# Kernel optimization log

Hardware: AMD Instinct MI355X
Metric: run time of the kernel (lower is better)

Reference implementation:

```python
import jax, jax.numpy as jnp
import numpy as np

T, B, H, V = 1024, 64, 256, 32000


def setup_inputs() -> dict:
    key = jax.random.key(0)
    ks = jax.random.split(key, 12)
    inputSequence = jax.random.randint(ks[0], (T, B), 0, V)
    lengths = jax.random.randint(ks[1], (B,), 1, T + 1)
    lengths = jnp.sort(lengths)[::-1]          # pack_padded_sequence needs descending
    lengths = lengths.at[0].set(T)             # max length == padded length
    s = 1.0 / np.sqrt(H)
    def w(k, shape):
        return jax.random.uniform(k, shape, jnp.float32, -s, s)
    return {
        "inputSequence": inputSequence,
        "inputLengths": lengths,
        "embedding": jax.random.normal(ks[2], (V, H), jnp.float32),
        "W_ih_f": w(ks[3], (3 * H, H)), "W_hh_f": w(ks[4], (3 * H, H)),
        "b_ih_f": w(ks[5], (3 * H,)),   "b_hh_f": w(ks[6], (3 * H,)),
        "W_ih_b": w(ks[7], (3 * H, H)), "W_hh_b": w(ks[8], (3 * H, H)),
        "b_ih_b": w(ks[9], (3 * H,)),   "b_hh_b": w(ks[10], (3 * H,)),
    }


def _gru_dir(emb, mask, Wih, Whh, bih, bhh, reverse):
    # emb: (T,B,H), mask: (T,B). PyTorch GRU cell math.
    Tn, Bn, Hn = emb.shape
    xg = emb @ Wih.T + bih                      # (T,B,3H) input-side gates precomputed
    def step(h, inp):
        xg_t, m = inp
        hg = h @ Whh.T + bhh                    # (B,3H)
        r = jax.nn.sigmoid(xg_t[:, :Hn] + hg[:, :Hn])
        z = jax.nn.sigmoid(xg_t[:, Hn:2 * Hn] + hg[:, Hn:2 * Hn])
        n = jnp.tanh(xg_t[:, 2 * Hn:] + r * hg[:, 2 * Hn:])
        h_new = (1.0 - z) * n + z * h
        m_ = m[:, None]
        h_next = jnp.where(m_, h_new, h)        # packed seq: frozen past length
        y = jnp.where(m_, h_new, 0.0)           # pad_packed zeros padded steps
        return h_next, y
    h0 = jnp.zeros((Bn, Hn), emb.dtype)
    hT, ys = jax.lax.scan(step, h0, (xg, mask), reverse=reverse)
    return ys, hT


def reference(inputSequence, inputLengths, embedding,
              W_ih_f, W_hh_f, b_ih_f, b_hh_f,
              W_ih_b, W_hh_b, b_ih_b, b_hh_b):
    Tn, Bn = inputSequence.shape
    emb = embedding[inputSequence]                              # (T,B,H)
    mask = jnp.arange(Tn)[:, None] < inputLengths[None, :]      # (T,B)
    yf, hf = _gru_dir(emb, mask, W_ih_f, W_hh_f, b_ih_f, b_hh_f, False)
    yb, hb = _gru_dir(emb, mask, W_ih_b, W_hh_b, b_ih_b, b_hh_b, True)
    outputs = yf + yb                                           # sum fwd/bwd halves
    hidden = jnp.stack([hf, hb], axis=0)                        # (2, B, H)
    return outputs, hidden
```

## Files before the change

kernel.cpp:

```cpp
#include <hip/hip_runtime.h>


typedef __attribute__((ext_vector_type(8))) short short8;
typedef __attribute__((ext_vector_type(4))) float floatx4;

__device__ __forceinline__ float rcp_(float x) { return __builtin_amdgcn_rcpf(x); }
__device__ __forceinline__ float sigmoid_(float x) { return rcp_(1.0f + __expf(-x)); }
__device__ __forceinline__ float tanh_(float x)    { return 1.0f - 2.0f * rcp_(1.0f + __expf(2.0f * x)); }
__device__ __forceinline__ unsigned short f2bf(float f) {
  unsigned int u = __float_as_uint(f);
  return (unsigned short)((u + 0x7fffu + ((u >> 16) & 1u)) >> 16);
}

__device__ __forceinline__ void ldsbar() {
  asm volatile("s_waitcnt lgkmcnt(0)" ::: "memory");
  __builtin_amdgcn_s_barrier();
  asm volatile("" ::: "memory");
}


__global__ __launch_bounds__(256) void prep_embB(
    const float* __restrict__ emb, unsigned short* __restrict__ embB) {
  int i4 = blockIdx.x * 256 + threadIdx.x;
  float4 v = ((const float4*)emb)[i4];
  ushort4 o;
  o.x = f2bf(v.x); o.y = f2bf(v.y); o.z = f2bf(v.z); o.w = f2bf(v.w);
  ((ushort4*)embB)[i4] = o;
}

__global__ __launch_bounds__(256) void prep_packB(
    const float* __restrict__ wf, const float* __restrict__ wb,
    unsigned short* __restrict__ oB) {
  int idx = blockIdx.x * 256 + threadIdx.x;
  int d = idx >= 196608;
  int o = idx - d * 196608;
  int jj   = o & 7;
  int lane = (o >> 3) & 63;
  int rest = o >> 9;
  int nt   = rest % 48;
  int kc   = rest / 48;
  int n = nt * 16 + (lane & 15);
  int k = kc * 32 + ((lane >> 4) << 3) + jj;
  const float* w = d ? wb : wf;
  oB[idx] = f2bf(w[n * 256 + k]);
}

__global__ __launch_bounds__(256) void prep_packA(
    const float* __restrict__ wf, const float* __restrict__ wb,
    unsigned short* __restrict__ oA) {
  int idx = blockIdx.x * 256 + threadIdx.x;
  int d = idx >= 196608;
  int o = idx - d * 196608;
  int jj   = o & 7;
  int lane = (o >> 3) & 63;
  int kc   = (o >> 9) & 7;
  int tl   = o >> 12;
  int row  = tl * 16 + (lane & 15);
  int k    = kc * 32 + ((lane >> 4) << 3) + jj;
  const float* w = d ? wb : wf;
  oA[idx] = f2bf(w[row * 256 + k]);
}

__global__ __launch_bounds__(512, 2) void fused_step(
    const int* __restrict__ seq, const int* __restrict__ lens,
    const unsigned short* __restrict__ embB,
    const unsigned short* __restrict__ pWihB,
    const unsigned short* __restrict__ pA,
    const float* __restrict__ bih_f, const float* __restrict__ bih_b,
    const float* __restrict__ bhh_f, const float* __restrict__ bhh_b,
    float* __restrict__ out, float* __restrict__ hcar,
    const float* __restrict__ xs_f, const float* __restrict__ xs_b,
    float* __restrict__ xw_f, float* __restrict__ xw_b,
    int nscan, int s_base_f, int s_base_b, int Tc, int is_last, int do_add,
    int xg_on, int x_base_f, int x_base_b) {
  __shared__ __align__(16) unsigned char smem[49152];
  const int bid = (int)blockIdx.x;
  const int tid = threadIdx.x;
  const int lane = tid & 63;

  if (bid < nscan) {
    __builtin_amdgcn_s_setprio(1);
    const int wv  = tid >> 6;
    const int qp  = bid >> 1;
    const int dir = bid & 1;
    const int b0  = qp * 2;

    const float* xg  = dir ? xs_b : xs_f;
    const float* bhh = dir ? bhh_b : bhh_f;
    const int len0 = lens[b0], len1 = lens[b0 + 1];
    const int lenmax = len0 > len1 ? len0 : len1;
    const int base = dir ? s_base_b : s_base_f;

    short8 af[6][8];
    {
      const short8* pA8 = (const short8*)(pA + (size_t)dir * 196608);
#pragma unroll
      for (int i = 0; i < 6; ++i) {
        const int tl = (i >> 1) * 16 + wv * 2 + (i & 1);
#pragma unroll
        for (int kc = 0; kc < 8; ++kc)
          af[i][kc] = pA8[((tl * 8 + kc) << 6) + lane];
      }
    }

    unsigned short* hbf = (unsigned short*)smem;
    float*          res = (float*)(smem + 2304);

    const int b  = lane >> 5;
    const int jj = lane & 31;
    const int j  = wv * 32 + jj;
    const int bb = b0 + b;
    const int blen = b ? len1 : len0;
    float hreg = hcar[dir * 16384 + bb * 256 + j];
    const float bhn = bhh[512 + j];
    hbf[b * 288 + j] = f2bf(hreg);
    __syncthreads();

    int s_lo, s_hi;
    if (dir == 0) { s_lo = 0; int e = lenmax - base; s_hi = e < 0 ? 0 : (e > Tc ? Tc : e); }
    else { int sk = base + Tc - lenmax; s_lo = sk < 0 ? 0 : (sk > Tc ? Tc : sk); s_hi = Tc; }

    const int nB = lane & 15, qq = lane >> 4;
    const bool bld = nB < 2;
    const unsigned short* hsrc0 = &hbf[nB * 288 + qq * 8];

    float xr = 0.f, xz = 0.f, xn = 0.f, oprev = 0.f;
    if (s_lo < s_hi) {
      const int t0  = dir ? (base + (Tc - 1 - s_lo)) : (base + s_lo);
      const float* xrow = xg + ((size_t)(t0 - base) * 64 + bb) * 768;
      xr = xrow[j]; xz = xrow[256 + j]; xn = xrow[512 + j];
      if (do_add) oprev = out[((size_t)t0 * 64 + bb) * 256 + j];
    }

    int p = 0;
    for (int s = s_lo; s < s_hi; ++s) {
      const int t  = dir ? (base + (Tc - 1 - s)) : (base + s);
      const bool act = t < blen;

      const int sn = (s + 1 < s_hi) ? s + 1 : s;
      const int tn = dir ? (base + (Tc - 1 - sn)) : (base + sn);
      float xr2, xz2, xn2, oprev2 = 0.f;
      {
        const float* xrow = xg + ((size_t)(tn - base) * 64 + bb) * 768;
        xr2 = xrow[j]; xz2 = xrow[256 + j]; xn2 = xrow[512 + j];
        if (do_add) oprev2 = out[((size_t)tn * 64 + bb) * 256 + j];
      }

      floatx4 acc[6];
#pragma unroll
      for (int i = 0; i < 6; ++i) acc[i] = (floatx4){0.f, 0.f, 0.f, 0.f};

      const unsigned short* hsrc = hsrc0 + p * 576;

      short8 b_cur = {0, 0, 0, 0, 0, 0, 0, 0};
      if (bld) b_cur = *(const short8*)(hsrc);
#pragma unroll
      for (int kc = 0; kc < 8; ++kc) {
        short8 b_nxt = {0, 0, 0, 0, 0, 0, 0, 0};
        if (kc < 7 && bld) b_nxt = *(const short8*)(hsrc + (kc + 1) * 32);
#pragma unroll
        for (int i = 0; i < 6; ++i)
          acc[i] = __builtin_amdgcn_mfma_f32_16x16x32_bf16(af[i][kc], b_cur, acc[i], 0, 0, 0);
        b_cur = b_nxt;
      }

      if (bld) {
#pragma unroll
        for (int i = 0; i < 6; ++i) {
          const int g = i >> 1, sub = i & 1;
          *(floatx4*)&res[(((wv * 3 + g) * 2 + nB) << 5) + sub * 16 + qq * 4] = acc[i];
        }
      }
      float ar = res[(((wv * 3 + 0) * 2 + b) << 5) + jj];
      float az = res[(((wv * 3 + 1) * 2 + b) << 5) + jj];
      float an = res[(((wv * 3 + 2) * 2 + b) << 5) + jj];

      float r  = sigmoid_(xr + ar);
      float z  = sigmoid_(xz + az);
      float nn = tanh_(xn + r * (an + bhn));
      float hn = (1.0f - z) * nn + z * hreg;
      if (act) hreg = hn;
      hbf[((p ^ 1) * 576) + b * 288 + j] = f2bf(hreg);
      if (act) out[((size_t)t * 64 + bb) * 256 + j] = do_add ? (oprev + hn) : hn;
      ldsbar();
      p ^= 1;

      xr = xr2; xz = xz2; xn = xn2; oprev = oprev2;
    }

    hcar[dir * 16384 + bb * 256 + j] = hreg;
    if (is_last)
      out[(size_t)1024 * 64 * 256 + (size_t)dir * 16384 + bb * 256 + j] = hreg;

  } else if (xg_on) {
    const int idx  = bid - nscan;
    const int sx   = idx >> 1;
    const int dir  = idx & 1;
    const int w    = tid >> 6;
    const int mt   = w & 3;
    const int h2   = w >> 2;
    const int t    = (dir ? x_base_b : x_base_f) + sx;
    const int c    = lane & 15, qq = lane >> 4;

    const float* bih = dir ? bih_b : bih_f;
    const float* bhh = dir ? bhh_b : bhh_f;
    float* xgo = (dir ? xw_b : xw_f) + (size_t)sx * 64 * 768;

    const int tk = seq[t * 64 + mt * 16 + c];
    const unsigned short* aptr = embB + (size_t)tk * 256 + qq * 8;
    short8 afr[8];
#pragma unroll
    for (int kc = 0; kc < 8; ++kc) afr[kc] = *(const short8*)(aptr + kc * 32);

    float4* Bs4 = (float4*)smem;

    floatx4 acc[24];
#pragma unroll
    for (int q = 0; q < 24; ++q) acc[q] = (floatx4){0.f, 0.f, 0.f, 0.f};

    for (int kc = 0; kc < 8; ++kc) {
      __syncthreads();
      const float4* src = (const float4*)(pWihB + (size_t)dir * 196608 + kc * 24576);
#pragma unroll
      for (int i = 0; i < 6; ++i) Bs4[tid + i * 512] = src[tid + i * 512];
      __syncthreads();
      const short8* bsv = (const short8*)Bs4;
      short8 af = afr[kc];
#pragma unroll
      for (int q = 0; q < 24; ++q) {
        int nt = h2 * 24 + q;
        acc[q] = __builtin_amdgcn_mfma_f32_16x16x32_bf16(af, bsv[nt * 64 + lane], acc[q], 0, 0, 0);
      }
    }

#pragma unroll
    for (int q = 0; q < 24; ++q) {
      int n = (h2 * 24 + q) * 16 + c;
      float bv = bih[n] + (n < 512 ? bhh[n] : 0.0f);
#pragma unroll
      for (int r = 0; r < 4; ++r)
        xgo[(size_t)(mt * 16 + qq * 4 + r) * 768 + n] = acc[q][r] + bv;
    }
  }
}

extern "C" void kernel_launch(void* const* d_in, const int* in_sizes, int n_in,
                              void* d_out, int out_size, void* d_ws, size_t ws_size,
                              hipStream_t stream) {
  const int*   seq   = (const int*)d_in[0];
  const int*   lens  = (const int*)d_in[1];
  const float* emb   = (const float*)d_in[2];
  const float* Wih_f = (const float*)d_in[3];
  const float* Whh_f = (const float*)d_in[4];
  const float* bih_f = (const float*)d_in[5];
  const float* bhh_f = (const float*)d_in[6];
  const float* Wih_b = (const float*)d_in[7];
  const float* Whh_b = (const float*)d_in[8];
  const float* bih_b = (const float*)d_in[9];
  const float* bhh_b = (const float*)d_in[10];
  float* out = (float*)d_out;
  float* ws  = (float*)d_ws;

  float*          hcar   = ws;
  unsigned short* pA     = (unsigned short*)(ws + 32768);
  unsigned short* pWihB  = (unsigned short*)(ws + 229376);
  unsigned short* embB   = (unsigned short*)(ws + 425984);
  float*          xgbase = ws + 4521984;

  int S[128], off[128], C = 0, Smax = 0;
  {
    size_t needA = (4521984ull + 4ull * 224ull * 49152ull) * 4ull;
    if (needA <= ws_size) {
      const int plan[6] = {64, 224, 224, 224, 224, 64};
      C = 6;
      for (int i = 0; i < C; ++i) S[i] = plan[i];
    } else {
      const int cands[7] = {512, 256, 128, 64, 32, 16, 8};
      int Tc = 8;
      for (int i = 0; i < 7; ++i) {
        size_t need = (4521984ull + 4ull * (size_t)cands[i] * 49152ull) * 4ull;
        if (need <= ws_size) { Tc = cands[i]; break; }
      }
      C = 1024 / Tc;
      for (int i = 0; i < C; ++i) S[i] = Tc;
    }
    int o = 0;
    for (int i = 0; i < C; ++i) { off[i] = o; o += S[i]; if (S[i] > Smax) Smax = S[i]; }
  }

  float* xb[2][2];
  for (int p = 0; p < 2; ++p)
    for (int d = 0; d < 2; ++d)
      xb[p][d] = xgbase + ((size_t)(p * 2 + d)) * Smax * 49152;

  hipMemsetAsync(d_out, 0, (size_t)1024 * 64 * 256 * 4, stream);
  hipMemsetAsync(hcar, 0, 32768ull * 4ull, stream);
  prep_embB<<<dim3(8000), dim3(256), 0, stream>>>(emb, embB);
  prep_packB<<<dim3(1536), dim3(256), 0, stream>>>(Wih_f, Wih_b, pWihB);
  prep_packA<<<dim3(1536), dim3(256), 0, stream>>>(Whh_f, Whh_b, pA);

  fused_step<<<dim3(2 * S[0]), dim3(512), 0, stream>>>(
      seq, lens, embB, pWihB, pA, bih_f, bih_b, bhh_f, bhh_b, out, hcar,
      xb[0][0], xb[0][1], xb[0][0], xb[0][1],
      0, 0, 0, S[0], 0, 0,
      1, off[0], off[C - 1]);

  for (int c = 0; c < C; ++c) {
    int xgon = (c + 1 < C) ? 1 : 0;
    int nblk = 64 + (xgon ? 2 * S[c + 1] : 0);
    fused_step<<<dim3(nblk), dim3(512), 0, stream>>>(
        seq, lens, embB, pWihB, pA, bih_f, bih_b, bhh_f, bhh_b, out, hcar,
        xb[c & 1][0], xb[c & 1][1], xb[(c + 1) & 1][0], xb[(c + 1) & 1][1],
        64, off[c], off[C - 1 - c], S[c],
        (c == C - 1) ? 1 : 0, (2 * c >= C) ? 1 : 0,
        xgon, xgon ? off[c + 1] : 0, xgon ? off[C - 2 - c] : 0);
  }
}
```

Before: 1.621 ms.

## Double block size to 1024 threads, halving per-wave MFMA work in scan and xg

Each fused_step block now has 16 waves. In the recurrent scan each wave owns 16 hidden units (3 gate tiles) instead of 32 (6 tiles), which shortens the serial MFMA chain per timestep and halves the resident Whh fragments per wave. Only half of each wave's lanes do the gate epilogue. The input-gate GEMM path splits its N tiles over more waves (12 accumulators instead of 24) and stages the B operand in fewer iterations. The trade-off is more waves syncing at the per-step barrier and idle lanes in the epilogue.

Measured after the change: 3.431 ms. +111.7%, slower.

```diff
diff --git a/kernel.cpp b/kernel.cpp
--- a/kernel.cpp
+++ b/kernel.cpp
@@ -61,7 +61,7 @@
   oA[idx] = f2bf(w[row * 256 + k]);
 }
 
-__global__ __launch_bounds__(512, 2) void fused_step(
+__global__ __launch_bounds__(1024, 4) void fused_step(
     const int* __restrict__ seq, const int* __restrict__ lens,
     const unsigned short* __restrict__ embB,
     const unsigned short* __restrict__ pWihB,
@@ -91,29 +91,31 @@
     const int lenmax = len0 > len1 ? len0 : len1;
     const int base = dir ? s_base_b : s_base_f;
 
-    short8 af[6][8];
+    short8 af[3][8];
     {
       const short8* pA8 = (const short8*)(pA + (size_t)dir * 196608);
 #pragma unroll
-      for (int i = 0; i < 6; ++i) {
-        const int tl = (i >> 1) * 16 + wv * 2 + (i & 1);
+      for (int g = 0; g < 3; ++g) {
+        const int tl = g * 16 + wv;
 #pragma unroll
         for (int kc = 0; kc < 8; ++kc)
-          af[i][kc] = pA8[((tl * 8 + kc) << 6) + lane];
+          af[g][kc] = pA8[((tl * 8 + kc) << 6) + lane];
       }
     }
 
     unsigned short* hbf = (unsigned short*)smem;
     float*          res = (float*)(smem + 2304);
 
-    const int b  = lane >> 5;
-    const int jj = lane & 31;
-    const int j  = wv * 32 + jj;
+    const bool epi = lane < 32;
+    const int b  = (lane >> 4) & 1;
+    const int jl = lane & 15;
+    const int j  = wv * 16 + jl;
     const int bb = b0 + b;
     const int blen = b ? len1 : len0;
-    float hreg = hcar[dir * 16384 + bb * 256 + j];
+    float hreg = 0.f;
+    if (epi) hreg = hcar[dir * 16384 + bb * 256 + j];
     const float bhn = bhh[512 + j];
-    hbf[b * 288 + j] = f2bf(hreg);
+    if (epi) hbf[b * 288 + j] = f2bf(hreg);
     __syncthreads();
 
     int s_lo, s_hi;
@@ -123,9 +125,10 @@
     const int nB = lane & 15, qq = lane >> 4;
     const bool bld = nB < 2;
     const unsigned short* hsrc0 = &hbf[nB * 288 + qq * 8];
+    const floatx4 ZERO4 = {0.f, 0.f, 0.f, 0.f};
 
     float xr = 0.f, xz = 0.f, xn = 0.f, oprev = 0.f;
-    if (s_lo < s_hi) {
+    if (epi && s_lo < s_hi) {
       const int t0  = dir ? (base + (Tc - 1 - s_lo)) : (base + s_lo);
       const float* xrow = xg + ((size_t)(t0 - base) * 64 + bb) * 768;
       xr = xrow[j]; xz = xrow[256 + j]; xn = xrow[512 + j];
@@ -139,58 +142,63 @@
 
       const int sn = (s + 1 < s_hi) ? s + 1 : s;
       const int tn = dir ? (base + (Tc - 1 - sn)) : (base + sn);
-      float xr2, xz2, xn2, oprev2 = 0.f;
-      {
+      float xr2 = 0.f, xz2 = 0.f, xn2 = 0.f, oprev2 = 0.f;
+      if (epi) {
         const float* xrow = xg + ((size_t)(tn - base) * 64 + bb) * 768;
         xr2 = xrow[j]; xz2 = xrow[256 + j]; xn2 = xrow[512 + j];
         if (do_add) oprev2 = out[((size_t)tn * 64 + bb) * 256 + j];
       }
 
-      floatx4 acc[6];
-#pragma unroll
-      for (int i = 0; i < 6; ++i) acc[i] = (floatx4){0.f, 0.f, 0.f, 0.f};
-
       const unsigned short* hsrc = hsrc0 + p * 576;
 
+      floatx4 acc[3];
       short8 b_cur = {0, 0, 0, 0, 0, 0, 0, 0};
       if (bld) b_cur = *(const short8*)(hsrc);
 #pragma unroll
       for (int kc = 0; kc < 8; ++kc) {
         short8 b_nxt = {0, 0, 0, 0, 0, 0, 0, 0};
         if (kc < 7 && bld) b_nxt = *(const short8*)(hsrc + (kc + 1) * 32);
-#pragma unroll
-        for (int i = 0; i < 6; ++i)
-          acc[i] = __builtin_amdgcn_mfma_f32_16x16x32_bf16(af[i][kc], b_cur, acc[i], 0, 0, 0);
+        if (kc == 0) {
+#pragma unroll
+          for (int g = 0; g < 3; ++g)
+            acc[g] = __builtin_amdgcn_mfma_f32_16x16x32_bf16(af[g][0], b_cur, ZERO4, 0, 0, 0);
+        } else {
+#pragma unroll
+          for (int g = 0; g < 3; ++g)
+            acc[g] = __builtin_amdgcn_mfma_f32_16x16x32_bf16(af[g][kc], b_cur, acc[g], 0, 0, 0);
+        }
         b_cur = b_nxt;
       }
 
       if (bld) {
 #pragma unroll
-        for (int i = 0; i < 6; ++i) {
-          const int g = i >> 1, sub = i & 1;
-          *(floatx4*)&res[(((wv * 3 + g) * 2 + nB) << 5) + sub * 16 + qq * 4] = acc[i];
-        }
-      }
-      float ar = res[(((wv * 3 + 0) * 2 + b) << 5) + jj];
-      float az = res[(((wv * 3 + 1) * 2 + b) << 5) + jj];
-      float an = res[(((wv * 3 + 2) * 2 + b) << 5) + jj];
-
-      float r  = sigmoid_(xr + ar);
-      float z  = sigmoid_(xz + az);
-      float nn = tanh_(xn + r * (an + bhn));
-      float hn = (1.0f - z) * nn + z * hreg;
-      if (act) hreg = hn;
-      hbf[((p ^ 1) * 576) + b * 288 + j] = f2bf(hreg);
-      if (act) out[((size_t)t * 64 + bb) * 256 + j] = do_add ? (oprev + hn) : hn;
+        for (int g = 0; g < 3; ++g)
+          *(floatx4*)&res[(((wv * 3 + g) * 2 + nB) << 4) + qq * 4] = acc[g];
+      }
+      float ar = res[(((wv * 3 + 0) * 2 + b) << 4) + jl];
+      float az = res[(((wv * 3 + 1) * 2 + b) << 4) + jl];
+      float an = res[(((wv * 3 + 2) * 2 + b) << 4) + jl];
+
+      if (epi) {
+        float r  = sigmoid_(xr + ar);
+        float z  = sigmoid_(xz + az);
+        float nn = tanh_(xn + r * (an + bhn));
+        float hn = (1.0f - z) * nn + z * hreg;
+        if (act) hreg = hn;
+        hbf[((p ^ 1) * 576) + b * 288 + j] = f2bf(hreg);
+        if (act) out[((size_t)t * 64 + bb) * 256 + j] = do_add ? (oprev + hn) : hn;
+      }
       ldsbar();
       p ^= 1;
 
       xr = xr2; xz = xz2; xn = xn2; oprev = oprev2;
     }
 
-    hcar[dir * 16384 + bb * 256 + j] = hreg;
-    if (is_last)
-      out[(size_t)1024 * 64 * 256 + (size_t)dir * 16384 + bb * 256 + j] = hreg;
+    if (epi) {
+      hcar[dir * 16384 + bb * 256 + j] = hreg;
+      if (is_last)
+        out[(size_t)1024 * 64 * 256 + (size_t)dir * 16384 + bb * 256 + j] = hreg;
+    }
 
   } else if (xg_on) {
     const int idx  = bid - nscan;
@@ -198,7 +206,7 @@
     const int dir  = idx & 1;
     const int w    = tid >> 6;
     const int mt   = w & 3;
-    const int h2   = w >> 2;
+    const int ng   = w >> 2;
     const int t    = (dir ? x_base_b : x_base_f) + sx;
     const int c    = lane & 15, qq = lane >> 4;
 
@@ -214,28 +222,28 @@
 
     float4* Bs4 = (float4*)smem;
 
-    floatx4 acc[24];
-#pragma unroll
-    for (int q = 0; q < 24; ++q) acc[q] = (floatx4){0.f, 0.f, 0.f, 0.f};
+    floatx4 acc[12];
+#pragma unroll
+    for (int q = 0; q < 12; ++q) acc[q] = (floatx4){0.f, 0.f, 0.f, 0.f};
 
     for (int kc = 0; kc < 8; ++kc) {
       __syncthreads();
       const float4* src = (const float4*)(pWihB + (size_t)dir * 196608 + kc * 24576);
 #pragma unroll
-      for (int i = 0; i < 6; ++i) Bs4[tid + i * 512] = src[tid + i * 512];
+      for (int i = 0; i < 3; ++i) Bs4[tid + i * 1024] = src[tid + i * 1024];
       __syncthreads();
       const short8* bsv = (const short8*)Bs4;
       short8 af = afr[kc];
 #pragma unroll
-      for (int q = 0; q < 24; ++q) {
-        int nt = h2 * 24 + q;
+      for (int q = 0; q < 12; ++q) {
+        int nt = ng * 12 + q;
         acc[q] = __builtin_amdgcn_mfma_f32_16x16x32_bf16(af, bsv[nt * 64 + lane], acc[q], 0, 0, 0);
       }
     }
 
 #pragma unroll
-    for (int q = 0; q < 24; ++q) {
-      int n = (h2 * 24 + q) * 16 + c;
+    for (int q = 0; q < 12; ++q) {
+      int n = (ng * 12 + q) * 16 + c;
       float bv = bih[n] + (n < 512 ? bhh[n] : 0.0f);
 #pragma unroll
       for (int r = 0; r < 4; ++r)
@@ -299,7 +307,7 @@
   prep_packB<<<dim3(1536), dim3(256), 0, stream>>>(Wih_f, Wih_b, pWihB);
   prep_packA<<<dim3(1536), dim3(256), 0, stream>>>(Whh_f, Whh_b, pA);
 
-  fused_step<<<dim3(2 * S[0]), dim3(512), 0, stream>>>(
+  fused_step<<<dim3(2 * S[0]), dim3(1024), 0, stream>>>(
       seq, lens, embB, pWihB, pA, bih_f, bih_b, bhh_f, bhh_b, out, hcar,
       xb[0][0], xb[0][1], xb[0][0], xb[0][1],
       0, 0, 0, S[0], 0, 0,
@@ -308,7 +316,7 @@
   for (int c = 0; c < C; ++c) {
     int xgon = (c + 1 < C) ? 1 : 0;
     int nblk = 64 + (xgon ? 2 * S[c + 1] : 0);
-    fused_step<<<dim3(nblk), dim3(512), 0, stream>>>(
+    fused_step<<<dim3(nblk), dim3(1024), 0, stream>>>(
         seq, lens, embB, pWihB, pA, bih_f, bih_b, bhh_f, bhh_b, out, hcar,
         xb[c & 1][0], xb[c & 1][1], xb[(c + 1) & 1][0], xb[(c + 1) & 1][1],
         64, off[c], off[C - 1 - c], S[c],
```
